# Optimization experiments

Hardware: AMD Instinct MI355X
Metric: run time of the kernel (lower is better)

Reference implementation:

```python
import jax, jax.numpy as jnp
import numpy as np

NP, P = 5, 5  # number of body parts, joints per part


def _windows(t):
    # (binf, length) for the 6 overlapping temporal windows of sequence()
    h, th = t // 2, t // 3
    return [(0, t), (0, h), (h, t - h), (0, th), (th, th), (2 * th, t - 2 * th)]


def _block(xw):
    # xw: (B, NP, P, L, C) -> Gaussian-embedding blocks (B, NP, L, C+1, C+1)
    B, n, p, L, C = xw.shape
    # smoothing over the P (joint-within-part) axis, as in the original code
    xs = xw.at[:, :, 1:-1].set((xw[:, :, 1:-1] + xw[:, :, :-2] + xw[:, :, 2:]) / 3)
    mu = xs.mean(axis=2)  # (B, NP, L, C)
    # temporally shifted centered slices (shifts over the L axis)
    x0 = xw - mu[:, :, None]                       # (B, NP, P, L, C)
    xm = xw[:, :, :, :-2] - mu[:, :, None, 1:-1]   # (B, NP, P, L-2, C)
    xp = xw[:, :, :, 2:] - mu[:, :, None, 1:-1]    # (B, NP, P, L-2, C)
    outer_mean = lambda a: jnp.einsum('bnptc,bnptd->bntcd', a, a) / p
    cov_mid = (outer_mean(xm) + outer_mean(x0[:, :, :, 1:-1]) + outer_mean(xp)) / 3
    xb = x0[:, :, :, ::L - 1]  # boundary frames 0 and L-1
    cov_b = jnp.einsum('bnptc,bnptd->bntcd', xb, xb) / p
    cov = jnp.zeros((B, n, L, C, C), xw.dtype)
    cov = cov.at[:, :, 1:-1].set(cov_mid)
    cov = cov.at[:, :, ::L - 1].set(cov_b)
    elt00 = cov + mu[..., :, None] * mu[..., None, :]  # cov + mu mu^T
    top = jnp.concatenate([elt00, mu[..., None]], axis=-1)            # (.., C, C+1)
    ones = jnp.ones((B, n, L, 1, 1), xw.dtype)
    bot = jnp.concatenate([mu[..., None, :], ones], axis=-1)          # (.., 1, C+1)
    return jnp.concatenate([top, bot], axis=-2)                        # (.., C+1, C+1)


def setup_inputs() -> dict:
    key = jax.random.key(0)
    x = jax.random.normal(key, (256, 600, 25, 3, 1), dtype=jnp.float32)
    return {"input": x}


def reference(input):
    B, T, J, C, _ = input.shape
    # (B, T, J, C, 1) -> (B, NP, P, T, C)  (matches transpose(1,2).reshape)
    x = jnp.moveaxis(input[..., 0], 1, 2).reshape(B, NP, P, T, C)
    blocks = [_block(x[:, :, :, b:b + L]) for b, L in _windows(T)]
    return jnp.concatenate(blocks, axis=2)  # (B, NP, sum(L_s), C+1, C+1)
```

## Files before the change

### kernel.cpp

```cpp
#include <hip/hip_runtime.h>


#define T_ 600
#define CH_ 50
#define NCH_ 12

typedef float fx4 __attribute__((ext_vector_type(4)));

#define BAR_LDS() do { asm volatile("s_waitcnt lgkmcnt(0)" ::: "memory"); \
                       __builtin_amdgcn_s_barrier(); } while (0)

__global__ __launch_bounds__(256) void gauss_agg_kernel(const float* __restrict__ x,
                                                        float* __restrict__ out) {
    __shared__ float raw[3908];
    __shared__ float4 obuf[256 * 5];

    int blk = blockIdx.x;
    int ch  = blk % NCH_;
    int b   = blk / NCH_;
    int tc  = ch * CH_;
    int tid = (int)threadIdx.x;

    int vtt = -1;
    switch (ch) {
        case 0:  vtt = 0;   break;
        case 3:  vtt = 199; break;
        case 4:  vtt = 200; break;
        case 5:  vtt = 299; break;
        case 6:  vtt = 300; break;
        case 7:  vtt = 399; break;
        case 8:  vtt = 400; break;
        case 11: vtt = 599; break;
        default: break;
    }

    int start = (tc == 0) ? 0 : tc - 1;
    int end   = tc + CH_ + 1; if (end > T_) end = T_;
    int nrows = end - start;
    int ofs   = tc - start;
    int tot   = nrows * 75;
    size_t gbase = (size_t)b * 45000 + (size_t)start * 75;

    int head = (int)((4 - (gbase & 3)) & 3);
    int off  = (4 - head) & 3;
    {
        if (head > tot) head = tot;
        int nv   = (tot - head) >> 2;
        int tail = tot - head - nv * 4;
        if (tid < head) raw[off + tid] = x[gbase + tid];
        const float4* srcv = reinterpret_cast<const float4*>(x + gbase + head);
        float4* rawv = reinterpret_cast<float4*>(&raw[off + head]);
        #pragma unroll
        for (int i = 0; i < 4; ++i) {
            int e = i * 256 + tid;
            if (e < nv) rawv[e] = srcv[e];
        }
        if (tid < tail) raw[off + head + 4 * nv + tid] = x[gbase + head + 4 * nv + tid];
    }
    BAR_LDS();

    {
        bool isvar = (tid >= 250);
        int n, tt;
        if (!isvar) { n = tid / 50; tt = tc + (tid - n * 50); }
        else        { int k = tid - 250; n = (k > 4) ? 4 : k; tt = (vtt < 0) ? tc : vtt; }
        int li = tt - tc + ofs;
        int lp = li - 1; if (lp < 0) lp = 0;
        int ln = li + 1;

        const float w5[5] = {4.f, 2.f, 3.f, 2.f, 4.f};
        const float* rc = &raw[off + li * 75 + n * 15];

        float s0=0.f,s1=0.f,s2=0.f, m0=0.f,m1=0.f,m2=0.f;
        float A00=0.f,A01=0.f,A02=0.f,A11=0.f,A12=0.f,A22=0.f;
        #pragma unroll
        for (int p = 0; p < 5; ++p) {
            float a = rc[p*3+0], c = rc[p*3+1], d = rc[p*3+2];
            s0 += a; s1 += c; s2 += d;
            m0 += w5[p]*a; m1 += w5[p]*c; m2 += w5[p]*d;
            A00 += a*a; A01 += a*c; A02 += a*d;
            A11 += c*c; A12 += c*d; A22 += d*d;
        }
        float mu0 = m0*(1.f/15.f), mu1 = m1*(1.f/15.f), mu2 = m2*(1.f/15.f);

        float inv = 0.2f;
        if (!isvar) {
            const float* r0 = &raw[off + lp * 75 + n * 15];
            const float* r1 = &raw[off + ln * 75 + n * 15];
            #pragma unroll
            for (int dstep = 0; dstep < 2; ++dstep) {
                const float* rn = dstep ? r1 : r0;
                #pragma unroll
                for (int p = 0; p < 5; ++p) {
                    float a = rn[p*3+0], c = rn[p*3+1], d = rn[p*3+2];
                    s0 += a; s1 += c; s2 += d;
                    A00 += a*a; A01 += a*c; A02 += a*d;
                    A11 += c*c; A12 += c*d; A22 += d*d;
                }
            }
            inv = 1.f/15.f;
        }

        float mb0 = s0*inv, mb1 = s1*inv, mb2 = s2*inv;
        float e00 = A00*inv - 2.f*mu0*mb0 + 2.f*mu0*mu0;
        float e01 = A01*inv - mu0*mb1 - mb0*mu1 + 2.f*mu0*mu1;
        float e02 = A02*inv - mu0*mb2 - mb0*mu2 + 2.f*mu0*mu2;
        float e11 = A11*inv - 2.f*mu1*mb1 + 2.f*mu1*mu1;
        float e12 = A12*inv - mu1*mb2 - mb1*mu2 + 2.f*mu1*mu2;
        float e22 = A22*inv - 2.f*mu2*mb2 + 2.f*mu2*mu2;

        int base = tid * 5;
        obuf[base + 0] = make_float4(e00, e01, e02, mu0);
        obuf[base + 1] = make_float4(e01, e11, e12, mu1);
        obuf[base + 2] = make_float4(e02, e12, e22, mu2);
        obuf[base + 3] = make_float4(mu0, mu1, mu2, 1.f);
    }
    BAR_LDS();

    fx4* outf4 = reinterpret_cast<fx4*>(out);
    #pragma unroll
    for (int k = 0; k < 12; ++k) {
        int f = k * 256 + tid;
        if (f < 3000) {
            int sl = f >> 2, pc = f & 3;
            int n  = sl / 150;
            int q  = sl - n * 150;
            int w  = q / 50;
            int tl = q - w * 50;
            int tt = tc + tl;
            bool bd;
            if (w == 0)      bd = (tt == 0) || (tt == 599);
            else if (w == 1) { int r = tt % 300; bd = (r == 0) || (r == 299); }
            else             { int r = tt % 200; bd = (r == 0) || (r == 199); }
            int oi = bd ? (250 + n) : sl % 250;
            if (!bd) oi = n * 50 + tl;
            size_t o = ((size_t)(b * 5 + n) * 1800 + w * 600 + tt) * 4 + pc;
            float4 v = obuf[oi * 5 + pc];
            fx4 nv; nv.x = v.x; nv.y = v.y; nv.z = v.z; nv.w = v.w;
            __builtin_nontemporal_store(nv, &outf4[o]);
        }
    }
}

extern "C" void kernel_launch(void* const* d_in, const int* in_sizes, int n_in,
                              void* d_out, int out_size, void* d_ws, size_t ws_size,
                              hipStream_t stream) {
    const float* x = (const float*)d_in[0];
    float* out = (float*)d_out;
    gauss_agg_kernel<<<256 * NCH_, 256, 0, stream>>>(x, out);
}
```

Baseline: 37.89 us.

## Make persistent blocks loop over four time chunks with register-prefetched input

The grid shrinks from 3072 to 768 blocks, and each block now processes four consecutive 50-frame chunks in a loop. While it computes and stores the current chunk, it prefetches the next chunk's input into registers, then copies it into LDS after the output stores. Chunk start rows are rounded down to a multiple of four, so global float4 loads are aligned and the head/tail handling is gone. This aims to overlap load latency with the store-heavy output phase, but it leaves only three blocks per CU and adds serialisation inside each block.

```diff
diff --git a/kernel.cpp b/kernel.cpp
--- a/kernel.cpp
+++ b/kernel.cpp
@@ -2,143 +2,159 @@
 
 
 #define T_ 600
-#define CH_ 50
-#define NCH_ 12
 
 typedef float fx4 __attribute__((ext_vector_type(4)));
 
 #define BAR_LDS() do { asm volatile("s_waitcnt lgkmcnt(0)" ::: "memory"); \
                        __builtin_amdgcn_s_barrier(); } while (0)
 
+__device__ __forceinline__ void chunkgeo(int tc, int& sp, int& tot) {
+    int s = (tc == 0) ? 0 : ((tc - 1) & ~3);
+    int e = tc + 51; if (e > T_) e = T_;
+    sp = s; tot = (e - s) * 75;
+}
+
 __global__ __launch_bounds__(256) void gauss_agg_kernel(const float* __restrict__ x,
                                                         float* __restrict__ out) {
-    __shared__ float raw[3908];
+    __shared__ float raw[4128];
     __shared__ float4 obuf[256 * 5];
 
     int blk = blockIdx.x;
-    int ch  = blk % NCH_;
-    int b   = blk / NCH_;
-    int tc  = ch * CH_;
+    int seg = blk % 3;
+    int b   = blk / 3;
     int tid = (int)threadIdx.x;
 
-    int vtt = -1;
-    switch (ch) {
-        case 0:  vtt = 0;   break;
-        case 3:  vtt = 199; break;
-        case 4:  vtt = 200; break;
-        case 5:  vtt = 299; break;
-        case 6:  vtt = 300; break;
-        case 7:  vtt = 399; break;
-        case 8:  vtt = 400; break;
-        case 11: vtt = 599; break;
-        default: break;
-    }
+    const float* xb = x + (size_t)b * 45000;
+    fx4* outf4 = reinterpret_cast<fx4*>(out);
+    const float w5[5] = {4.f, 2.f, 3.f, 2.f, 4.f};
+    float4* rawv = reinterpret_cast<float4*>(raw);
 
-    int start = (tc == 0) ? 0 : tc - 1;
-    int end   = tc + CH_ + 1; if (end > T_) end = T_;
-    int nrows = end - start;
-    int ofs   = tc - start;
-    int tot   = nrows * 75;
-    size_t gbase = (size_t)b * 45000 + (size_t)start * 75;
+    float4 v[5]; float vt = 0.f;
 
-    int head = (int)((4 - (gbase & 3)) & 3);
-    int off  = (4 - head) & 3;
     {
-        if (head > tot) head = tot;
-        int nv   = (tot - head) >> 2;
-        int tail = tot - head - nv * 4;
-        if (tid < head) raw[off + tid] = x[gbase + tid];
-        const float4* srcv = reinterpret_cast<const float4*>(x + gbase + head);
-        float4* rawv = reinterpret_cast<float4*>(&raw[off + head]);
+        int sp, tot; chunkgeo(seg * 200, sp, tot);
+        int nv = tot >> 2, tail = tot & 3;
+        const float4* srcv = reinterpret_cast<const float4*>(xb + (size_t)sp * 75);
         #pragma unroll
-        for (int i = 0; i < 4; ++i) {
-            int e = i * 256 + tid;
-            if (e < nv) rawv[e] = srcv[e];
-        }
-        if (tid < tail) raw[off + head + 4 * nv + tid] = x[gbase + head + 4 * nv + tid];
+        for (int i = 0; i < 5; ++i) { int e = i * 256 + tid; if (e < nv) v[i] = srcv[e]; }
+        if (tid < tail) vt = xb[(size_t)sp * 75 + nv * 4 + tid];
+        #pragma unroll
+        for (int i = 0; i < 5; ++i) { int e = i * 256 + tid; if (e < nv) rawv[e] = v[i]; }
+        if (tid < tail) raw[nv * 4 + tid] = vt;
     }
     BAR_LDS();
 
-    {
-        bool isvar = (tid >= 250);
-        int n, tt;
-        if (!isvar) { n = tid / 50; tt = tc + (tid - n * 50); }
-        else        { int k = tid - 250; n = (k > 4) ? 4 : k; tt = (vtt < 0) ? tc : vtt; }
-        int li = tt - tc + ofs;
-        int lp = li - 1; if (lp < 0) lp = 0;
-        int ln = li + 1;
+    for (int c = 0; c < 4; ++c) {
+        int tc = seg * 200 + c * 50;
+        int cg = tc / 50;
 
-        const float w5[5] = {4.f, 2.f, 3.f, 2.f, 4.f};
-        const float* rc = &raw[off + li * 75 + n * 15];
-
-        float s0=0.f,s1=0.f,s2=0.f, m0=0.f,m1=0.f,m2=0.f;
-        float A00=0.f,A01=0.f,A02=0.f,A11=0.f,A12=0.f,A22=0.f;
-        #pragma unroll
-        for (int p = 0; p < 5; ++p) {
-            float a = rc[p*3+0], c = rc[p*3+1], d = rc[p*3+2];
-            s0 += a; s1 += c; s2 += d;
-            m0 += w5[p]*a; m1 += w5[p]*c; m2 += w5[p]*d;
-            A00 += a*a; A01 += a*c; A02 += a*d;
-            A11 += c*c; A12 += c*d; A22 += d*d;
-        }
-        float mu0 = m0*(1.f/15.f), mu1 = m1*(1.f/15.f), mu2 = m2*(1.f/15.f);
-
-        float inv = 0.2f;
-        if (!isvar) {
-            const float* r0 = &raw[off + lp * 75 + n * 15];
-            const float* r1 = &raw[off + ln * 75 + n * 15];
-            #pragma unroll
-            for (int dstep = 0; dstep < 2; ++dstep) {
-                const float* rn = dstep ? r1 : r0;
-                #pragma unroll
-                for (int p = 0; p < 5; ++p) {
-                    float a = rn[p*3+0], c = rn[p*3+1], d = rn[p*3+2];
-                    s0 += a; s1 += c; s2 += d;
-                    A00 += a*a; A01 += a*c; A02 += a*d;
-                    A11 += c*c; A12 += c*d; A22 += d*d;
-                }
-            }
-            inv = 1.f/15.f;
+        int vtt = -1;
+        switch (cg) {
+            case 0:  vtt = 0;   break;  case 3:  vtt = 199; break;
+            case 4:  vtt = 200; break;  case 5:  vtt = 299; break;
+            case 6:  vtt = 300; break;  case 7:  vtt = 399; break;
+            case 8:  vtt = 400; break;  case 11: vtt = 599; break;
+            default: break;
         }
 
-        float mb0 = s0*inv, mb1 = s1*inv, mb2 = s2*inv;
-        float e00 = A00*inv - 2.f*mu0*mb0 + 2.f*mu0*mu0;
-        float e01 = A01*inv - mu0*mb1 - mb0*mu1 + 2.f*mu0*mu1;
-        float e02 = A02*inv - mu0*mb2 - mb0*mu2 + 2.f*mu0*mu2;
-        float e11 = A11*inv - 2.f*mu1*mb1 + 2.f*mu1*mu1;
-        float e12 = A12*inv - mu1*mb2 - mb1*mu2 + 2.f*mu1*mu2;
-        float e22 = A22*inv - 2.f*mu2*mb2 + 2.f*mu2*mu2;
+        int sp, tot; chunkgeo(tc, sp, tot);
+        int lofs = tc - sp;
 
-        int base = tid * 5;
-        obuf[base + 0] = make_float4(e00, e01, e02, mu0);
-        obuf[base + 1] = make_float4(e01, e11, e12, mu1);
-        obuf[base + 2] = make_float4(e02, e12, e22, mu2);
-        obuf[base + 3] = make_float4(mu0, mu1, mu2, 1.f);
-    }
-    BAR_LDS();
+        int nsp = 0, ntot = 0, nnv = 0, ntail = 0;
+        if (c < 3) {
+            chunkgeo(tc + 50, nsp, ntot);
+            nnv = ntot >> 2; ntail = ntot & 3;
+            const float4* srcv = reinterpret_cast<const float4*>(xb + (size_t)nsp * 75);
+            #pragma unroll
+            for (int i = 0; i < 5; ++i) { int e = i * 256 + tid; if (e < nnv) v[i] = srcv[e]; }
+            if (tid < ntail) vt = xb[(size_t)nsp * 75 + nnv * 4 + tid];
+        }
 
-    fx4* outf4 = reinterpret_cast<fx4*>(out);
-    #pragma unroll
-    for (int k = 0; k < 12; ++k) {
-        int f = k * 256 + tid;
-        if (f < 3000) {
-            int sl = f >> 2, pc = f & 3;
-            int n  = sl / 150;
-            int q  = sl - n * 150;
-            int w  = q / 50;
-            int tl = q - w * 50;
-            int tt = tc + tl;
-            bool bd;
-            if (w == 0)      bd = (tt == 0) || (tt == 599);
-            else if (w == 1) { int r = tt % 300; bd = (r == 0) || (r == 299); }
-            else             { int r = tt % 200; bd = (r == 0) || (r == 199); }
-            int oi = bd ? (250 + n) : sl % 250;
-            if (!bd) oi = n * 50 + tl;
-            size_t o = ((size_t)(b * 5 + n) * 1800 + w * 600 + tt) * 4 + pc;
-            float4 v = obuf[oi * 5 + pc];
-            fx4 nv; nv.x = v.x; nv.y = v.y; nv.z = v.z; nv.w = v.w;
-            __builtin_nontemporal_store(nv, &outf4[o]);
+        {
+            bool isvar = (tid >= 250);
+            int n, tt;
+            if (!isvar) { n = tid / 50; tt = tc + (tid - n * 50); }
+            else        { int k = tid - 250; n = (k > 4) ? 4 : k; tt = (vtt < 0) ? tc : vtt; }
+            int li = (tt - tc) + lofs;
+            int lp = li - 1; if (lp < 0) lp = 0;
+            int ln = li + 1;
+
+            const float* rc = &raw[li * 75 + n * 15];
+
+            float s0=0.f,s1=0.f,s2=0.f, m0=0.f,m1=0.f,m2=0.f;
+            float A00=0.f,A01=0.f,A02=0.f,A11=0.f,A12=0.f,A22=0.f;
+            #pragma unroll
+            for (int p = 0; p < 5; ++p) {
+                float a = rc[p*3+0], cc = rc[p*3+1], d = rc[p*3+2];
+                s0 += a; s1 += cc; s2 += d;
+                m0 += w5[p]*a; m1 += w5[p]*cc; m2 += w5[p]*d;
+                A00 += a*a; A01 += a*cc; A02 += a*d;
+                A11 += cc*cc; A12 += cc*d; A22 += d*d;
+            }
+            float mu0 = m0*(1.f/15.f), mu1 = m1*(1.f/15.f), mu2 = m2*(1.f/15.f);
+
+            float inv = 0.2f;
+            if (!isvar) {
+                const float* r0 = &raw[lp * 75 + n * 15];
+                const float* r1 = &raw[ln * 75 + n * 15];
+                #pragma unroll
+                for (int dstep = 0; dstep < 2; ++dstep) {
+                    const float* rn = dstep ? r1 : r0;
+                    #pragma unroll
+                    for (int p = 0; p < 5; ++p) {
+                        float a = rn[p*3+0], cc = rn[p*3+1], d = rn[p*3+2];
+                        s0 += a; s1 += cc; s2 += d;
+                        A00 += a*a; A01 += a*cc; A02 += a*d;
+                        A11 += cc*cc; A12 += cc*d; A22 += d*d;
+                    }
+                }
+                inv = 1.f/15.f;
+            }
+
+            float mb0 = s0*inv, mb1 = s1*inv, mb2 = s2*inv;
+            float e00 = A00*inv - 2.f*mu0*mb0 + 2.f*mu0*mu0;
+            float e01 = A01*inv - mu0*mb1 - mb0*mu1 + 2.f*mu0*mu1;
+            float e02 = A02*inv - mu0*mb2 - mb0*mu2 + 2.f*mu0*mu2;
+            float e11 = A11*inv - 2.f*mu1*mb1 + 2.f*mu1*mu1;
+            float e12 = A12*inv - mu1*mb2 - mb1*mu2 + 2.f*mu1*mu2;
+            float e22 = A22*inv - 2.f*mu2*mb2 + 2.f*mu2*mu2;
+
+            int base = tid * 5;
+            obuf[base + 0] = make_float4(e00, e01, e02, mu0);
+            obuf[base + 1] = make_float4(e01, e11, e12, mu1);
+            obuf[base + 2] = make_float4(e02, e12, e22, mu2);
+            obuf[base + 3] = make_float4(mu0, mu1, mu2, 1.f);
         }
+        BAR_LDS();
+
+        #pragma unroll
+        for (int k = 0; k < 12; ++k) {
+            int f = k * 256 + tid;
+            if (f < 3000) {
+                int sl = f >> 2, pc = f & 3;
+                int n  = sl / 150;
+                int q  = sl - n * 150;
+                int w  = q / 50;
+                int tl = q - w * 50;
+                int tt = tc + tl;
+                bool bd;
+                if (w == 0)      bd = (tt == 0) || (tt == 599);
+                else if (w == 1) { int r = tt % 300; bd = (r == 0) || (r == 299); }
+                else             { int r = tt % 200; bd = (r == 0) || (r == 199); }
+                int oi = bd ? (250 + n) : (n * 50 + tl);
+                size_t o = ((size_t)(b * 5 + n) * 1800 + w * 600 + tt) * 4 + pc;
+                float4 vv = obuf[oi * 5 + pc];
+                fx4 nv4; nv4.x = vv.x; nv4.y = vv.y; nv4.z = vv.z; nv4.w = vv.w;
+                __builtin_nontemporal_store(nv4, &outf4[o]);
+            }
+        }
+
+        if (c < 3) {
+            #pragma unroll
+            for (int i = 0; i < 5; ++i) { int e = i * 256 + tid; if (e < nnv) rawv[e] = v[i]; }
+            if (tid < ntail) raw[nnv * 4 + tid] = vt;
+        }
+        BAR_LDS();
     }
 }
 
@@ -147,5 +163,5 @@
                               hipStream_t stream) {
     const float* x = (const float*)d_in[0];
     float* out = (float*)d_out;
-    gauss_agg_kernel<<<256 * NCH_, 256, 0, stream>>>(x, out);
+    gauss_agg_kernel<<<768, 256, 0, stream>>>(x, out);
 }
```

New measurement: 54.19 us. 43.0% more time.
